# Optimization experiments

Measured on AMD Instinct MI355X. Metric: run time of the kernel, lower is better.

The kernel has to match this reference:

```python
import jax, jax.numpy as jnp
import numpy as np

K_TOP = 64  # top-k selection size (init kwarg k)


def setup_inputs() -> dict:
    key = jax.random.key(0)
    k1, k2, k3, k4 = jax.random.split(key, 4)
    N, M, D = 512, 100000, 1024
    queries = jax.random.normal(k1, (N, D), dtype=jnp.float32)
    keys = jax.random.normal(k2, (M, D), dtype=jnp.float32)
    values = jax.random.normal(k3, (M, D), dtype=jnp.float32)
    affine = jax.random.normal(k4, (D,), dtype=jnp.float32)  # diag affine param (low_parameter=True)
    return {"queries": queries, "keys": keys, "values": values, "affine": affine}


def reference(queries, keys, values, affine):
    # low_parameter=True -> weight matrix is diag(affine): (queries @ diag(a)) == queries * a
    # scores[n, m] = (queries * affine) @ keys.T ; reduce max over queries dim (dim=0)
    scores = jnp.max(jnp.einsum('nd,md->nm', queries * affine, keys), axis=0)  # [M]
    weights, indices = jax.lax.top_k(scores, K_TOP)            # [k], [k]
    w = jax.nn.softmax(weights)                                # softmax over the k selected scores
    encoding = jnp.sum(w[:, None] * values[indices], axis=0)   # [V]
    return encoding, indices
```

## Files before the change

kernel.cpp:

```cpp
#include <hip/hip_runtime.h>
#include <cstdint>
#include <cstddef>


typedef __attribute__((ext_vector_type(8))) short bf16x8;
typedef __attribute__((ext_vector_type(4))) float f32x4;

static constexpr int NQ = 512;
static constexpr int DD = 1024;
static constexpr int MK = 100000;
static constexpr int BM = 64;
static constexpr int BK = 64;
static constexpr int NKS = DD / BK;
static constexpr int MBLOCKS = (MK + BM - 1) / BM;
static constexpr int CAP = 1024;

static constexpr size_t KSTAGE_OFF   = 0;
static constexpr size_t KSTAGE_BYTES = (size_t)MBLOCKS * NKS * BM * 128;
static constexpr size_t QSTAGE_OFF   = KSTAGE_OFF + KSTAGE_BYTES;
static constexpr size_t QSTAGE_BYTES = (size_t)NKS * NQ * 128;
static constexpr size_t SCORES_OFF   = QSTAGE_OFF + QSTAGE_BYTES;
static constexpr size_t SCORES_BYTES = (size_t)MBLOCKS * BM * sizeof(float);
static constexpr size_t CIDX_OFF     = SCORES_OFF + SCORES_BYTES;
static constexpr size_t RESC_OFF     = CIDX_OFF + (size_t)CAP * 4;
static constexpr size_t CNT_OFF      = RESC_OFF + (size_t)CAP * 4;
static constexpr size_t HIST_OFF     = CNT_OFF + 64;
static constexpr size_t VLO_OFF      = HIST_OFF + 8192 * 4;

static constexpr int AOFF = 0;
static constexpr int BOFF = 8192;
static constexpr int GEMM_LDS = 8192 + 65536;

static __device__ __forceinline__ unsigned short f32_to_bf16_rne(float f) {
    unsigned int u = __float_as_uint(f);
    unsigned int r = (u + 0x7FFFu + ((u >> 16) & 1u)) >> 16;
    return (unsigned short)r;
}
static __device__ __forceinline__ unsigned int xform(float f) {
    unsigned int u = __float_as_uint(f);
    return u ^ ((unsigned int)((int)u >> 31) | 0x80000000u);
}
static __device__ __forceinline__ float unxform(unsigned int u) {
    unsigned int b = (u & 0x80000000u) ? (u ^ 0x80000000u) : ~u;
    return __uint_as_float(b);
}

typedef __attribute__((address_space(1))) const unsigned int g1u32;
typedef __attribute__((address_space(3))) unsigned int l3u32;
static __device__ __forceinline__ void async16(const void* g, void* l) {
    __builtin_amdgcn_global_load_lds((g1u32*)g, (l3u32*)(uintptr_t)l, 16, 0, 0);
}

__global__ void prep_q(const float* __restrict__ q, const float* __restrict__ a,
                       unsigned short* __restrict__ qs) {
    int id  = blockIdx.x * 256 + threadIdx.x;
    int p   = id & 7;
    int row = (id >> 3) & (NQ - 1);
    int ks  = id >> 12;
    int c   = p ^ (row & 7);
    int kb  = ks * BK + c * 8;

    const float* qrow = q + (size_t)row * DD + kb;
    float4 v0 = *(const float4*)(qrow);
    float4 v1 = *(const float4*)(qrow + 4);
    float4 a0 = *(const float4*)(a + kb);
    float4 a1 = *(const float4*)(a + kb + 4);
    float f[8] = {v0.x * a0.x, v0.y * a0.y, v0.z * a0.z, v0.w * a0.w,
                  v1.x * a1.x, v1.y * a1.y, v1.z * a1.z, v1.w * a1.w};
    bf16x8 o;
#pragma unroll
    for (int j = 0; j < 8; ++j) o[j] = (short)f32_to_bf16_rne(f[j]);
    *(bf16x8*)(qs + (size_t)id * 8) = o;
}

__global__ void prep_keys(const float* __restrict__ keys,
                          unsigned short* __restrict__ kst) {
    size_t id = (size_t)blockIdx.x * 256 + threadIdx.x;
    int p   = (int)(id & 7);
    int row = (int)((id >> 3) & 63);
    int ks  = (int)((id >> 9) & 15);
    int mb  = (int)(id >> 13);
    int gm  = mb * 64 + row;
    bf16x8 o;
    if (gm < MK) {
        int col = ks * BK + (p ^ (row & 7)) * 8;
        const float* src = keys + (size_t)gm * DD + col;
        float4 v0 = *(const float4*)(src);
        float4 v1 = *(const float4*)(src + 4);
        float f[8] = {v0.x, v0.y, v0.z, v0.w, v1.x, v1.y, v1.z, v1.w};
#pragma unroll
        for (int j = 0; j < 8; ++j) o[j] = (short)f32_to_bf16_rne(f[j]);
    } else {
#pragma unroll
        for (int j = 0; j < 8; ++j) o[j] = 0;
    }
    *(bf16x8*)(kst + id * 8) = o;
}

__launch_bounds__(512, 4)
__global__ void scores_gemm(const unsigned short* __restrict__ kstage,
                            const unsigned short* __restrict__ qs,
                            float* __restrict__ scores) {
    extern __shared__ char smem[];
    const int tid  = threadIdx.x;
    const int wid  = tid >> 6;
    const int lane = tid & 63;
    const int g    = lane >> 4;
    const int r16  = lane & 15;

    const int nwg = gridDim.x;
    const int qq  = nwg >> 3, rr = nwg & 7;
    const int xcd = blockIdx.x & 7, loc = blockIdx.x >> 3;
    const int mb  = (xcd < rr ? xcd * (qq + 1) : rr * (qq + 1) + (xcd - rr) * qq) + loc;
    const int m0  = mb * BM;

    const char* asrc = (const char*)kstage + ((size_t)mb * NKS) * 8192
                     + wid * 1024 + lane * 16;
    const char* bsrc = (const char*)qs + (size_t)(wid * 64) * 128 + (size_t)lane * 16;

    int aoff[2][4], boff[2][4];
#pragma unroll
    for (int s = 0; s < 2; ++s) {
#pragma unroll
        for (int rt = 0; rt < 4; ++rt) {
            int row = rt * 16 + r16;
            aoff[s][rt] = AOFF + row * 128 + (((s * 4 + g) ^ (row & 7)) << 4);
        }
#pragma unroll
        for (int ct = 0; ct < 4; ++ct) {
            int row = wid * 64 + ct * 16 + r16;
            boff[s][ct] = BOFF + row * 128 + (((s * 4 + g) ^ (row & 7)) << 4);
        }
    }

    f32x4 acc[4][4] = {};

    for (int ks = 0; ks < NKS; ++ks) {
        async16(asrc + (size_t)ks * 8192, smem + AOFF + wid * 1024);
#pragma unroll
        for (int i = 0; i < 8; ++i)
            async16(bsrc + (size_t)ks * 65536 + i * 1024,
                    smem + BOFF + wid * 8192 + i * 1024);
        __syncthreads();

#pragma unroll
        for (int s = 0; s < 2; ++s) {
            bf16x8 ah[4], bh[4];
#pragma unroll
            for (int rt = 0; rt < 4; ++rt) ah[rt] = *(const bf16x8*)(smem + aoff[s][rt]);
#pragma unroll
            for (int ct = 0; ct < 4; ++ct) bh[ct] = *(const bf16x8*)(smem + boff[s][ct]);
#pragma unroll
            for (int rt = 0; rt < 4; ++rt)
#pragma unroll
                for (int ct = 0; ct < 4; ++ct)
                    acc[rt][ct] = __builtin_amdgcn_mfma_f32_16x16x32_bf16(ah[rt], bh[ct], acc[rt][ct], 0, 0, 0);
        }
        __syncthreads();
    }

    float* wmax = (float*)smem;
#pragma unroll
    for (int rt = 0; rt < 4; ++rt) {
#pragma unroll
        for (int r = 0; r < 4; ++r) {
            float mx = acc[rt][0][r];
            mx = fmaxf(mx, acc[rt][1][r]);
            mx = fmaxf(mx, acc[rt][2][r]);
            mx = fmaxf(mx, acc[rt][3][r]);
#pragma unroll
            for (int off = 1; off < 16; off <<= 1)
                mx = fmaxf(mx, __shfl_xor(mx, off));
            if (r16 == 0) wmax[wid * 64 + rt * 16 + g * 4 + r] = mx;
        }
    }
    __syncthreads();
    if (tid < BM) {
        float mx = wmax[tid];
#pragma unroll
        for (int w = 1; w < 8; ++w) mx = fmaxf(mx, wmax[w * 64 + tid]);
        int gm = m0 + tid;
        if (gm < MK) scores[gm] = mx;
    }
}

__global__ void zero_hist(unsigned int* __restrict__ hist, int* __restrict__ cnt) {
    int i = blockIdx.x * 1024 + threadIdx.x;
    if (i < 8192) hist[i] = 0;
    if (i == 0) cnt[0] = 0;
}

__global__ void hist_build(const float* __restrict__ scores, unsigned int* __restrict__ hist) {
    __shared__ unsigned int lh[8192];
    for (int i = threadIdx.x; i < 8192; i += 256) lh[i] = 0;
    __syncthreads();
    for (int i = blockIdx.x * 256 + threadIdx.x; i < MK; i += gridDim.x * 256)
        atomicAdd(&lh[xform(scores[i]) >> 19], 1u);
    __syncthreads();
    for (int i = threadIdx.x; i < 8192; i += 256) {
        unsigned int c = lh[i];
        if (c) atomicAdd(&hist[i], c);
    }
}

__launch_bounds__(1024)
__global__ void find_thresh(const unsigned int* __restrict__ hist, float* __restrict__ vlo) {
    __shared__ unsigned int s0[1024], s1[1024];
    const int tid = threadIdx.x;
    unsigned int s = 0;
#pragma unroll
    for (int j = 0; j < 8; ++j) s += hist[tid * 8 + j];
    s0[tid] = s;
    __syncthreads();
    unsigned int* src = s0;
    unsigned int* dst = s1;
    for (int off = 1; off < 1024; off <<= 1) {
        unsigned int v = src[tid] + ((tid + off < 1024) ? src[tid + off] : 0u);
        __syncthreads();
        dst[tid] = v;
        __syncthreads();
        unsigned int* t = src; src = dst; dst = t;
    }
    unsigned int suf  = src[tid];
    unsigned int sufn = (tid < 1023) ? src[tid + 1] : 0u;
    if (suf >= 64u && sufn < 64u) {
        unsigned int acc = sufn;
        int b = tid * 8 + 7;
        for (;; --b) { acc += hist[b]; if (acc >= 64u) break; }
        vlo[0] = unxform(((unsigned int)b) << 19) - 1.0f;
    }
}

__global__ void collect(const float* __restrict__ scores, const float* __restrict__ vlo,
                        int* __restrict__ cidx, int* __restrict__ cnt) {
    const float t = vlo[0];
    for (int i = blockIdx.x * 256 + threadIdx.x; i < MK; i += gridDim.x * 256) {
        if (scores[i] >= t) {
            int p = atomicAdd(cnt, 1);
            if (p < CAP) cidx[p] = i;
        }
    }
}

__launch_bounds__(256)
__global__ void rescore(const float* __restrict__ q, const float* __restrict__ a,
                        const float* __restrict__ keys,
                        const int* __restrict__ cidx, const int* __restrict__ cnt,
                        float* __restrict__ resc) {
    __shared__ float w[1024];
    __shared__ float smax[4];
    const int b = blockIdx.x;
    if (b >= cnt[0]) return;
    const int m   = cidx[b];
    const int tid = threadIdx.x;

    for (int d = tid; d < 1024; d += 256) w[d] = a[d] * keys[(size_t)m * DD + d];
    __syncthreads();

    const int wid = tid >> 6, lane = tid & 63;
    float best = -__builtin_inff();
    for (int n = wid; n < NQ; n += 4) {
        const float* qr = q + (size_t)n * DD;
        float p = 0.f;
#pragma unroll
        for (int j = 0; j < 4; ++j) {
            float4 v  = *(const float4*)(qr + lane * 4 + 256 * j);
            float4 ww = *(const float4*)(&w[lane * 4 + 256 * j]);
            p += v.x * ww.x + v.y * ww.y + v.z * ww.z + v.w * ww.w;
        }
#pragma unroll
        for (int off = 1; off < 64; off <<= 1) p += __shfl_xor(p, off);
        best = fmaxf(best, p);
    }
    if (lane == 0) smax[wid] = best;
    __syncthreads();
    if (tid == 0)
        resc[b] = fmaxf(fmaxf(smax[0], smax[1]), fmaxf(smax[2], smax[3]));
}

__launch_bounds__(256)
__global__ void final_select(const int* __restrict__ cidx, const float* __restrict__ resc,
                             const int* __restrict__ cnt, const float* __restrict__ values,
                             float* __restrict__ out) {
    __shared__ float selw[64];
    __shared__ int   seli[64];
    const int tid = threadIdx.x;
    int nc = cnt[0];
    if (nc > CAP) nc = CAP;

    if (tid < 64) {
        const int lane = tid;
        float lv[16]; int li[16];
#pragma unroll
        for (int j = 0; j < 16; ++j) {
            int slot = lane + 64 * j;
            bool ok = slot < nc;
            lv[j] = ok ? resc[slot] : -__builtin_inff();
            li[j] = ok ? cidx[slot] : 0x7fffffff;
        }
        for (int it = 0; it < 64; ++it) {
            float bv = -__builtin_inff();
            int bg = 0x7fffffff, bj = 0;
#pragma unroll
            for (int j = 0; j < 16; ++j)
                if (lv[j] > bv || (lv[j] == bv && li[j] < bg)) { bv = lv[j]; bg = li[j]; bj = j; }
            int bcode = (lane << 4) | bj;
#pragma unroll
            for (int off = 1; off < 64; off <<= 1) {
                float ov = __shfl_xor(bv, off);
                int   og = __shfl_xor(bg, off);
                int   oc = __shfl_xor(bcode, off);
                if (ov > bv || (ov == bv && og < bg)) { bv = ov; bg = og; bcode = oc; }
            }
            if ((bcode >> 4) == lane) {
                int wj = bcode & 15;
#pragma unroll
                for (int j = 0; j < 16; ++j) if (j == wj) lv[j] = -__builtin_inff();
            }
            if (lane == 0) { selw[it] = bv; seli[it] = bg; }
        }
    }
    __syncthreads();

    if (tid < 64) {
        float x = selw[tid];
        float mx = x;
#pragma unroll
        for (int off = 1; off < 64; off <<= 1) mx = fmaxf(mx, __shfl_xor(mx, off));
        float e = expf(x - mx);
        float s = e;
#pragma unroll
        for (int off = 1; off < 64; off <<= 1) s += __shfl_xor(s, off);
        selw[tid] = e / s;
        out[DD + tid] = (float)seli[tid];
    }
    __syncthreads();

    for (int d = tid; d < DD; d += 256) {
        float accv = 0.f;
        for (int i = 0; i < 64; ++i)
            accv += selw[i] * values[(size_t)seli[i] * DD + d];
        out[d] = accv;
    }
}

extern "C" void kernel_launch(void* const* d_in, const int* in_sizes, int n_in,
                              void* d_out, int out_size, void* d_ws, size_t ws_size,
                              hipStream_t stream) {
    (void)in_sizes; (void)n_in; (void)out_size; (void)ws_size;
    const float* queries = (const float*)d_in[0];
    const float* keys    = (const float*)d_in[1];
    const float* values  = (const float*)d_in[2];
    const float* affine  = (const float*)d_in[3];
    float* out = (float*)d_out;
    char*  ws  = (char*)d_ws;

    unsigned short* kstage = (unsigned short*)(ws + KSTAGE_OFF);
    unsigned short* qstage = (unsigned short*)(ws + QSTAGE_OFF);
    float* scores = (float*)(ws + SCORES_OFF);
    int*   cidx   = (int*)(ws + CIDX_OFF);
    float* resc   = (float*)(ws + RESC_OFF);
    int*   cnt    = (int*)(ws + CNT_OFF);
    unsigned int* hist = (unsigned int*)(ws + HIST_OFF);
    float* vlo    = (float*)(ws + VLO_OFF);

    hipFuncSetAttribute((const void*)scores_gemm,
                        hipFuncAttributeMaxDynamicSharedMemorySize, GEMM_LDS);

    prep_q<<<(NKS * NQ * 8) / 256, 256, 0, stream>>>(queries, affine, qstage);
    prep_keys<<<(MBLOCKS * NKS * BM * 8) / 256, 256, 0, stream>>>(keys, kstage);
    scores_gemm<<<MBLOCKS, 512, GEMM_LDS, stream>>>(kstage, qstage, scores);
    zero_hist<<<8, 1024, 0, stream>>>(hist, cnt);
    hist_build<<<64, 256, 0, stream>>>(scores, hist);
    find_thresh<<<1, 1024, 0, stream>>>(hist, vlo);
    collect<<<200, 256, 0, stream>>>(scores, vlo, cidx, cnt);
    rescore<<<CAP, 256, 0, stream>>>(queries, affine, keys, cidx, cnt, resc);
    final_select<<<1, 256, 0, stream>>>(cidx, resc, cnt, values, out);
}
```

Baseline: 534.5 us.

## Double-buffer GEMM LDS with 32-wide K slices and coalesced key staging

The scores GEMM now uses 32-wide K steps with two LDS buffers, prefetching the next slice while running MFMAs on the current one, and raises wave priority around the MFMA block. Staging layouts for keys and queries change to a 64-byte row swizzle to match. prep_keys now reads full contiguous key rows, transposes them through 128KB of LDS per block, and writes the staged tile out contiguously, aiming for better coalescing. The costs are more loop iterations with a barrier each, and the large LDS in prep_keys, which limits occupancy to one block per CU.

```diff
diff --git a/kernel.cpp b/kernel.cpp
--- a/kernel.cpp
+++ b/kernel.cpp
@@ -10,15 +10,14 @@
 static constexpr int DD = 1024;
 static constexpr int MK = 100000;
 static constexpr int BM = 64;
-static constexpr int BK = 64;
-static constexpr int NKS = DD / BK;
+static constexpr int NKK = DD / 32;
 static constexpr int MBLOCKS = (MK + BM - 1) / BM;
 static constexpr int CAP = 1024;
 
 static constexpr size_t KSTAGE_OFF   = 0;
-static constexpr size_t KSTAGE_BYTES = (size_t)MBLOCKS * NKS * BM * 128;
+static constexpr size_t KSTAGE_BYTES = (size_t)MBLOCKS * 131072;
 static constexpr size_t QSTAGE_OFF   = KSTAGE_OFF + KSTAGE_BYTES;
-static constexpr size_t QSTAGE_BYTES = (size_t)NKS * NQ * 128;
+static constexpr size_t QSTAGE_BYTES = (size_t)NKK * NQ * 64;
 static constexpr size_t SCORES_OFF   = QSTAGE_OFF + QSTAGE_BYTES;
 static constexpr size_t SCORES_BYTES = (size_t)MBLOCKS * BM * sizeof(float);
 static constexpr size_t CIDX_OFF     = SCORES_OFF + SCORES_BYTES;
@@ -29,7 +28,8 @@
 
 static constexpr int AOFF = 0;
 static constexpr int BOFF = 8192;
-static constexpr int GEMM_LDS = 8192 + 65536;
+static constexpr int GEMM_LDS = 8192 + 2 * 32768;
+static constexpr int PREP_LDS = 131072;
 
 static __device__ __forceinline__ unsigned short f32_to_bf16_rne(float f) {
     unsigned int u = __float_as_uint(f);
@@ -54,11 +54,10 @@
 __global__ void prep_q(const float* __restrict__ q, const float* __restrict__ a,
                        unsigned short* __restrict__ qs) {
     int id  = blockIdx.x * 256 + threadIdx.x;
-    int p   = id & 7;
-    int row = (id >> 3) & (NQ - 1);
-    int ks  = id >> 12;
-    int c   = p ^ (row & 7);
-    int kb  = ks * BK + c * 8;
+    int c   = id & 3;
+    int row = (id >> 2) & (NQ - 1);
+    int kk  = id >> 11;
+    int kb  = kk * 32 + ((c ^ (row & 3)) << 3);
 
     const float* qrow = q + (size_t)row * DD + kb;
     float4 v0 = *(const float4*)(qrow);
@@ -73,28 +72,43 @@
     *(bf16x8*)(qs + (size_t)id * 8) = o;
 }
 
+__launch_bounds__(1024)
 __global__ void prep_keys(const float* __restrict__ keys,
                           unsigned short* __restrict__ kst) {
-    size_t id = (size_t)blockIdx.x * 256 + threadIdx.x;
-    int p   = (int)(id & 7);
-    int row = (int)((id >> 3) & 63);
-    int ks  = (int)((id >> 9) & 15);
-    int mb  = (int)(id >> 13);
-    int gm  = mb * 64 + row;
-    bf16x8 o;
-    if (gm < MK) {
-        int col = ks * BK + (p ^ (row & 7)) * 8;
-        const float* src = keys + (size_t)gm * DD + col;
-        float4 v0 = *(const float4*)(src);
-        float4 v1 = *(const float4*)(src + 4);
-        float f[8] = {v0.x, v0.y, v0.z, v0.w, v1.x, v1.y, v1.z, v1.w};
-#pragma unroll
-        for (int j = 0; j < 8; ++j) o[j] = (short)f32_to_bf16_rne(f[j]);
-    } else {
-#pragma unroll
-        for (int j = 0; j < 8; ++j) o[j] = 0;
-    }
-    *(bf16x8*)(kst + id * 8) = o;
+    extern __shared__ char lds[];
+    const int mb = blockIdx.x;
+    const int t  = threadIdx.x;
+    const int col8 = t & 127;
+    const int rsub = t >> 7;
+
+#pragma unroll
+    for (int it = 0; it < 8; ++it) {
+        const int row = it * 8 + rsub;
+        const int gm  = mb * 64 + row;
+        bf16x8 o;
+        if (gm < MK) {
+            const float* src = keys + (size_t)gm * DD + col8 * 8;
+            float4 v0 = *(const float4*)(src);
+            float4 v1 = *(const float4*)(src + 4);
+            float f[8] = {v0.x, v0.y, v0.z, v0.w, v1.x, v1.y, v1.z, v1.w};
+#pragma unroll
+            for (int j = 0; j < 8; ++j) o[j] = (short)f32_to_bf16_rne(f[j]);
+        } else {
+#pragma unroll
+            for (int j = 0; j < 8; ++j) o[j] = 0;
+        }
+        const int ks = col8 >> 2;
+        const int c  = col8 & 3;
+        *(bf16x8*)(lds + ks * 4096 + row * 64 + (((c ^ (row & 3))) << 4)) = o;
+    }
+    __syncthreads();
+
+    char* dst = (char*)kst + (size_t)mb * 131072;
+#pragma unroll
+    for (int it = 0; it < 8; ++it) {
+        const int off = it * 16384 + t * 16;
+        *(f32x4*)(dst + off) = *(const f32x4*)(lds + off);
+    }
 }
 
 __launch_bounds__(512, 4)
@@ -114,48 +128,50 @@
     const int mb  = (xcd < rr ? xcd * (qq + 1) : rr * (qq + 1) + (xcd - rr) * qq) + loc;
     const int m0  = mb * BM;
 
-    const char* asrc = (const char*)kstage + ((size_t)mb * NKS) * 8192
-                     + wid * 1024 + lane * 16;
-    const char* bsrc = (const char*)qs + (size_t)(wid * 64) * 128 + (size_t)lane * 16;
-
-    int aoff[2][4], boff[2][4];
-#pragma unroll
-    for (int s = 0; s < 2; ++s) {
-#pragma unroll
-        for (int rt = 0; rt < 4; ++rt) {
-            int row = rt * 16 + r16;
-            aoff[s][rt] = AOFF + row * 128 + (((s * 4 + g) ^ (row & 7)) << 4);
-        }
-#pragma unroll
-        for (int ct = 0; ct < 4; ++ct) {
-            int row = wid * 64 + ct * 16 + r16;
-            boff[s][ct] = BOFF + row * 128 + (((s * 4 + g) ^ (row & 7)) << 4);
-        }
-    }
+    const char* asrc = (const char*)kstage + (size_t)mb * 131072
+                     + (wid & 3) * 1024 + lane * 16;
+    const char* bsrc = (const char*)qs + (size_t)(wid * 64) * 64 + (size_t)lane * 16;
+    const int   bdst = BOFF + wid * 4096;
+    const int   adst = AOFF + (wid & 3) * 1024;
+
+    const int sw = ((g ^ (r16 & 3)) << 4);
+    int arow_rd[4], brow_rd[4];
+#pragma unroll
+    for (int rt = 0; rt < 4; ++rt) arow_rd[rt] = AOFF + (rt * 16 + r16) * 64 + sw;
+#pragma unroll
+    for (int ct = 0; ct < 4; ++ct) brow_rd[ct] = BOFF + (wid * 64 + ct * 16 + r16) * 64 + sw;
 
     f32x4 acc[4][4] = {};
 
-    for (int ks = 0; ks < NKS; ++ks) {
-        async16(asrc + (size_t)ks * 8192, smem + AOFF + wid * 1024);
-#pragma unroll
-        for (int i = 0; i < 8; ++i)
-            async16(bsrc + (size_t)ks * 65536 + i * 1024,
-                    smem + BOFF + wid * 8192 + i * 1024);
-        __syncthreads();
-
-#pragma unroll
-        for (int s = 0; s < 2; ++s) {
-            bf16x8 ah[4], bh[4];
-#pragma unroll
-            for (int rt = 0; rt < 4; ++rt) ah[rt] = *(const bf16x8*)(smem + aoff[s][rt]);
-#pragma unroll
-            for (int ct = 0; ct < 4; ++ct) bh[ct] = *(const bf16x8*)(smem + boff[s][ct]);
-#pragma unroll
-            for (int rt = 0; rt < 4; ++rt)
-#pragma unroll
-                for (int ct = 0; ct < 4; ++ct)
-                    acc[rt][ct] = __builtin_amdgcn_mfma_f32_16x16x32_bf16(ah[rt], bh[ct], acc[rt][ct], 0, 0, 0);
-        }
+    if (wid < 4) async16(asrc, smem + adst);
+#pragma unroll
+    for (int i = 0; i < 4; ++i)
+        async16(bsrc + i * 1024, smem + bdst + i * 1024);
+    __syncthreads();
+
+    for (int ks = 0; ks < NKK; ++ks) {
+        const int cur = ks & 1, nxt = cur ^ 1;
+        if (ks + 1 < NKK) {
+            if (wid < 4) async16(asrc + (size_t)(ks + 1) * 4096, smem + nxt * 4096 + adst);
+#pragma unroll
+            for (int i = 0; i < 4; ++i)
+                async16(bsrc + (size_t)(ks + 1) * 32768 + i * 1024,
+                        smem + nxt * 32768 + bdst + i * 1024);
+        }
+        bf16x8 ah[4], bh[4];
+#pragma unroll
+        for (int rt = 0; rt < 4; ++rt)
+            ah[rt] = *(const bf16x8*)(smem + cur * 4096 + arow_rd[rt]);
+#pragma unroll
+        for (int ct = 0; ct < 4; ++ct)
+            bh[ct] = *(const bf16x8*)(smem + cur * 32768 + brow_rd[ct]);
+        __builtin_amdgcn_s_setprio(1);
+#pragma unroll
+        for (int rt = 0; rt < 4; ++rt)
+#pragma unroll
+            for (int ct = 0; ct < 4; ++ct)
+                acc[rt][ct] = __builtin_amdgcn_mfma_f32_16x16x32_bf16(ah[rt], bh[ct], acc[rt][ct], 0, 0, 0);
+        __builtin_amdgcn_s_setprio(0);
         __syncthreads();
     }
 
@@ -366,9 +382,11 @@
 
     hipFuncSetAttribute((const void*)scores_gemm,
                         hipFuncAttributeMaxDynamicSharedMemorySize, GEMM_LDS);
-
-    prep_q<<<(NKS * NQ * 8) / 256, 256, 0, stream>>>(queries, affine, qstage);
-    prep_keys<<<(MBLOCKS * NKS * BM * 8) / 256, 256, 0, stream>>>(keys, kstage);
+    hipFuncSetAttribute((const void*)prep_keys,
+                        hipFuncAttributeMaxDynamicSharedMemorySize, PREP_LDS);
+
+    prep_q<<<(NKK * NQ * 4) / 256, 256, 0, stream>>>(queries, affine, qstage);
+    prep_keys<<<MBLOCKS, 1024, PREP_LDS, stream>>>(keys, kstage);
     scores_gemm<<<MBLOCKS, 512, GEMM_LDS, stream>>>(kstage, qstage, scores);
     zero_hist<<<8, 1024, 0, stream>>>(hist, cnt);
     hist_build<<<64, 256, 0, stream>>>(scores, hist);
```

Measured after the change: 538.8 us. About the same (+0.8%).
